# Performance work log

Hardware: AMD Instinct MI355X
Metric: run time of the kernel (lower is better)

## Reference

```python
import jax, jax.numpy as jnp
import numpy as np

D_MODEL = 1024
NUM_HEADS = 16
HEAD_DIM = D_MODEL // NUM_HEADS
ALPHA = 1.0


def setup_inputs() -> dict:
    key = jax.random.key(0)
    ks = jax.random.split(key, 9)
    B, T, D = 2, 2048, D_MODEL
    s = 1.0 / np.sqrt(D)
    inp = {
        "x": jax.random.normal(ks[0], (B, T, D), dtype=jnp.float32),
        "Wq": jax.random.uniform(ks[1], (D, D), jnp.float32, -s, s),
        "bq": jax.random.uniform(ks[2], (D,), jnp.float32, -s, s),
        "Wk": jax.random.uniform(ks[3], (D, D), jnp.float32, -s, s),
        "bk": jax.random.uniform(ks[4], (D,), jnp.float32, -s, s),
        "Wv": jax.random.uniform(ks[5], (D, D), jnp.float32, -s, s),
        "bv": jax.random.uniform(ks[6], (D,), jnp.float32, -s, s),
        "Wo": jax.random.uniform(ks[7], (D, D), jnp.float32, -s, s),
        "bo": jax.random.uniform(ks[8], (D,), jnp.float32, -s, s),
    }
    return inp


def reference(x, Wq, bq, Wk, bk, Wv, bv, Wo, bo):
    B, T, D = x.shape
    H, hd = NUM_HEADS, HEAD_DIM

    def split_heads(y):  # [B,T,D] -> [B,H,T,hd]
        return y.reshape(B, T, H, hd).transpose(0, 2, 1, 3)

    Q = split_heads(x @ Wq.T + bq)
    K = split_heads(x @ Wk.T + bk)
    V = split_heads(x @ Wv.T + bv)

    scores = jnp.einsum('bhid,bhjd->bhij', Q, K) / jnp.sqrt(jnp.float32(hd))

    t = jnp.arange(T)
    delta = t[:, None] - t[None, :]  # [T,T], i - j
    causal_mask = delta < 0          # j > i (strict upper triangle)
    # similarity_power_law decay bias: -(delta)^alpha for delta >= 0, else 0
    decay = jnp.where(causal_mask, 0.0, -(delta.astype(jnp.float32) ** ALPHA))

    scores = jnp.where(causal_mask, -jnp.inf, scores) + decay
    attn = jax.nn.softmax(scores, axis=-1)

    out = jnp.einsum('bhij,bhjd->bhid', attn, V)
    out = out.transpose(0, 2, 1, 3).reshape(B, T, D)
    return out @ Wo.T + bo
```

## Files before the change

### kernel.cpp

```cpp
#include <hip/hip_runtime.h>

#define TT 2048
#define DD 1024
#define HH 16
#define HD 64
#define NTOK 4096

typedef __bf16 bf16x8 __attribute__((ext_vector_type(8)));
typedef short short4v __attribute__((ext_vector_type(4)));
typedef float f32x4 __attribute__((ext_vector_type(4)));

__device__ __forceinline__ unsigned short f2bf(float f) {
  unsigned u = __float_as_uint(f);
  u += 0x7fffu + ((u >> 16) & 1u);
  return (unsigned short)(u >> 16);
}

#if __has_builtin(__builtin_amdgcn_mfma_f32_16x16x16bf16_1k)
__device__ __forceinline__ f32x4 mfma16(short4v a, short4v b, f32x4 c) {
  return __builtin_amdgcn_mfma_f32_16x16x16bf16_1k(a, b, c, 0, 0, 0);
}
#else
__device__ __forceinline__ f32x4 mfma16(short4v a, short4v b, f32x4 c) {
  asm("v_mfma_f32_16x16x16_bf16 %0, %1, %2, %0\n\ts_nop 7\n\ts_nop 7"
      : "+v"(c) : "v"(a), "v"(b));
  return c;
}
#endif

typedef void __attribute__((address_space(1))) as1_void;
typedef void __attribute__((address_space(3))) as3_void;
__device__ __forceinline__ void gl_lds16(const void* g, void* l) {
  __builtin_amdgcn_global_load_lds((as1_void*)g, (as3_void*)l, 16, 0, 0);
}

__global__ void wcmha_cast_bf16(const float4* __restrict__ src,
                                ushort4* __restrict__ dst, int n4) {
  int i = blockIdx.x * blockDim.x + threadIdx.x;
  if (i < n4) {
    float4 v = src[i];
    ushort4 o;
    o.x = f2bf(v.x); o.y = f2bf(v.y); o.z = f2bf(v.z); o.w = f2bf(v.w);
    dst[i] = o;
  }
}

#define BM 128
#define BN 64
#define BK 32

template <int MODE>
__global__ __launch_bounds__(256)
void wcmha_gemm(const unsigned short* __restrict__ X,
                const unsigned short* __restrict__ W,
                const float* __restrict__ bias,
                void* __restrict__ Y) {
  __shared__ unsigned short As[BM * BK];
  __shared__ unsigned short Bs[BN * BK];
  const int tid = threadIdx.x;
  const int wid = tid >> 6;
  const int lane = tid & 63;
  const int m = lane & 15, quad = lane >> 4;
  const int m0 = blockIdx.x * BM;
  const int n0 = blockIdx.y * BN;
  const int wm = (wid >> 1) * 64;
  const int wn = (wid & 1) * 32;

  const int ca0 = wid * 128 + lane;
  const int ca1 = ca0 + 64;
  const int cb  = wid * 64 + lane;
  const unsigned short* aga = X + (size_t)(m0 + (ca0 >> 2)) * DD + (ca0 & 3) * 8;
  const unsigned short* agb = X + (size_t)(m0 + (ca1 >> 2)) * DD + (ca1 & 3) * 8;
  const unsigned short* bga = W + (size_t)(n0 + (cb >> 2)) * DD + (cb & 3) * 8;
  unsigned short* lda = &As[wid * 1024];
  unsigned short* ldb = &As[wid * 1024 + 512];
  unsigned short* ldc = &Bs[wid * 512];

  f32x4 acc[4][2];
#pragma unroll
  for (int i = 0; i < 4; ++i)
#pragma unroll
    for (int j = 0; j < 2; ++j) acc[i][j] = (f32x4){0.f, 0.f, 0.f, 0.f};

  for (int k0 = 0; k0 < DD; k0 += BK) {
    gl_lds16(aga + k0, lda);
    gl_lds16(agb + k0, ldb);
    gl_lds16(bga + k0, ldc);
    __syncthreads();
    bf16x8 af[4], bf[2];
#pragma unroll
    for (int mi = 0; mi < 4; ++mi)
      af[mi] = *(const bf16x8*)&As[(wm + mi * 16 + m) * BK + quad * 8];
#pragma unroll
    for (int ni = 0; ni < 2; ++ni)
      bf[ni] = *(const bf16x8*)&Bs[(wn + ni * 16 + m) * BK + quad * 8];
#pragma unroll
    for (int mi = 0; mi < 4; ++mi)
#pragma unroll
      for (int ni = 0; ni < 2; ++ni)
        acc[mi][ni] = (MODE == 1)
            ? __builtin_amdgcn_mfma_f32_16x16x32_bf16(bf[ni], af[mi], acc[mi][ni], 0, 0, 0)
            : __builtin_amdgcn_mfma_f32_16x16x32_bf16(af[mi], bf[ni], acc[mi][ni], 0, 0, 0);
    __syncthreads();
  }

  if (MODE == 2) {
    float* dst = (float*)Y;
#pragma unroll
    for (int mi = 0; mi < 4; ++mi)
#pragma unroll
      for (int ni = 0; ni < 2; ++ni) {
        int col = n0 + wn + ni * 16 + m;
        float bb = bias[col];
#pragma unroll
        for (int r = 0; r < 4; ++r) {
          int row = m0 + wm + mi * 16 + quad * 4 + r;
          dst[(size_t)row * DD + col] = acc[mi][ni][r] + bb;
        }
      }
  } else if (MODE == 0) {
    unsigned short* dst = (unsigned short*)Y;
#pragma unroll
    for (int mi = 0; mi < 4; ++mi)
#pragma unroll
      for (int ni = 0; ni < 2; ++ni) {
        int col = n0 + wn + ni * 16 + m;
        int h = col >> 6, d = col & 63;
        float bb = bias[col];
#pragma unroll
        for (int r = 0; r < 4; ++r) {
          int row = m0 + wm + mi * 16 + quad * 4 + r;
          int b = row >> 11, t = row & (TT - 1);
          dst[((size_t)(b * HH + h) * TT + t) * HD + d] = f2bf(acc[mi][ni][r] + bb);
        }
      }
  } else {
    unsigned short* dst = (unsigned short*)Y;
#pragma unroll
    for (int mi = 0; mi < 4; ++mi)
#pragma unroll
      for (int ni = 0; ni < 2; ++ni) {
        int row = m0 + wm + mi * 16 + m;
        int b = row >> 11, t = row & (TT - 1);
#pragma unroll
        for (int r = 0; r < 4; ++r) {
          int col = n0 + wn + ni * 16 + quad * 4 + r;
          int h = col >> 6, d = col & 63;
          dst[((size_t)(b * HH + h) * HD + d) * TT + t] = f2bf(acc[mi][ni][r] + bias[col]);
        }
      }
  }
}

__global__ __launch_bounds__(256)
void wcmha_attn(const unsigned short* __restrict__ Qb,
                const unsigned short* __restrict__ Kb,
                const unsigned short* __restrict__ Vt,
                unsigned short* __restrict__ O) {
  const int wid = threadIdx.x >> 6, lane = threadIdx.x & 63;
  const int gw = (blockIdx.x << 2) + wid;
  const int qt = gw & 127, bh = gw >> 7;
  const int qbase = qt << 4;
  const int il = lane & 15, quad = lane >> 4;
  const int ig = qbase + il;

  const unsigned short* q_ptr = Qb + (size_t)bh * TT * HD;
  const unsigned short* k_ptr = Kb + (size_t)bh * TT * HD;
  const unsigned short* v_ptr = Vt + (size_t)bh * HD * TT;

  const bf16x8 qf0 = *(const bf16x8*)(q_ptr + (size_t)ig * HD + quad * 8);
  const bf16x8 qf1 = *(const bf16x8*)(q_ptr + (size_t)ig * HD + 32 + quad * 8);

  const int j0 = (qbase >= 48) ? qbase - 48 : 0;

  f32x4 st[4];
#pragma unroll
  for (int jt = 0; jt < 4; ++jt) {
    const unsigned short* kp = k_ptr + (size_t)(j0 + jt * 16 + il) * HD;
    bf16x8 k0 = *(const bf16x8*)(kp + quad * 8);
    bf16x8 k1 = *(const bf16x8*)(kp + 32 + quad * 8);
    f32x4 a = {0.f, 0.f, 0.f, 0.f};
    a = __builtin_amdgcn_mfma_f32_16x16x32_bf16(k0, qf0, a, 0, 0, 0);
    a = __builtin_amdgcn_mfma_f32_16x16x32_bf16(k1, qf1, a, 0, 0, 0);
    st[jt] = a;
  }

  float mloc = -3.0e38f;
#pragma unroll
  for (int jt = 0; jt < 4; ++jt)
#pragma unroll
    for (int r = 0; r < 4; ++r) {
      int jg = j0 + jt * 16 + quad * 4 + r;
      float v = (jg > ig) ? -3.0e38f : st[jt][r] * 0.125f - (float)(ig - jg);
      st[jt][r] = v;
      mloc = fmaxf(mloc, v);
    }
  mloc = fmaxf(mloc, __shfl_xor(mloc, 16));
  mloc = fmaxf(mloc, __shfl_xor(mloc, 32));

  float rs = 0.f;
  short4v pf[4];
#pragma unroll
  for (int jt = 0; jt < 4; ++jt)
#pragma unroll
    for (int r = 0; r < 4; ++r) {
      float p = __expf(st[jt][r] - mloc);
      rs += p;
      pf[jt][r] = (short)f2bf(p);
    }
  rs += __shfl_xor(rs, 16);
  rs += __shfl_xor(rs, 32);

  f32x4 o_acc[4];
#pragma unroll
  for (int nt = 0; nt < 4; ++nt) o_acc[nt] = (f32x4){0.f, 0.f, 0.f, 0.f};
#pragma unroll
  for (int jt = 0; jt < 4; ++jt)
#pragma unroll
    for (int nt = 0; nt < 4; ++nt) {
      short4v vf = *(const short4v*)(v_ptr + (size_t)(nt * 16 + il) * TT +
                                     j0 + jt * 16 + quad * 4);
      o_acc[nt] = mfma16(vf, pf[jt], o_acc[nt]);
    }

  const float inv_l = 1.f / rs;
  const int b = bh >> 4, hh = bh & 15;
  unsigned short* ob = O + ((size_t)(b * TT + ig)) * DD + hh * HD;
#pragma unroll
  for (int nt = 0; nt < 4; ++nt)
#pragma unroll
    for (int r = 0; r < 4; ++r)
      ob[nt * 16 + quad * 4 + r] = f2bf(o_acc[nt][r] * inv_l);
}

extern "C" void kernel_launch(void* const* d_in, const int* in_sizes, int n_in,
                              void* d_out, int out_size, void* d_ws, size_t ws_size,
                              hipStream_t stream) {
  const float* x  = (const float*)d_in[0];
  const float* Wq = (const float*)d_in[1];
  const float* bq = (const float*)d_in[2];
  const float* Wk = (const float*)d_in[3];
  const float* bk = (const float*)d_in[4];
  const float* Wv = (const float*)d_in[5];
  const float* bv = (const float*)d_in[6];
  const float* Wo = (const float*)d_in[7];
  const float* bo = (const float*)d_in[8];

  char* ws = (char*)d_ws;
  unsigned short* xb  = (unsigned short*)(ws);
  unsigned short* wqb = (unsigned short*)(ws + (8u << 20));
  unsigned short* wkb = wqb + (1u << 20);
  unsigned short* wvb = wkb + (1u << 20);
  unsigned short* wob = wvb + (1u << 20);
  unsigned short* Qb  = (unsigned short*)(ws + (16u << 20));
  unsigned short* Kb  = (unsigned short*)(ws + (24u << 20));
  unsigned short* Vt  = (unsigned short*)(ws + (32u << 20));
  unsigned short* Ob  = xb;

  wcmha_cast_bf16<<<4096, 256, 0, stream>>>((const float4*)x,  (ushort4*)xb,  NTOK * DD / 4);
  wcmha_cast_bf16<<<1024, 256, 0, stream>>>((const float4*)Wq, (ushort4*)wqb, DD * DD / 4);
  wcmha_cast_bf16<<<1024, 256, 0, stream>>>((const float4*)Wk, (ushort4*)wkb, DD * DD / 4);
  wcmha_cast_bf16<<<1024, 256, 0, stream>>>((const float4*)Wv, (ushort4*)wvb, DD * DD / 4);
  wcmha_cast_bf16<<<1024, 256, 0, stream>>>((const float4*)Wo, (ushort4*)wob, DD * DD / 4);

  dim3 gproj(NTOK / BM, DD / BN);
  wcmha_gemm<0><<<gproj, 256, 0, stream>>>(xb, wqb, bq, Qb);
  wcmha_gemm<0><<<gproj, 256, 0, stream>>>(xb, wkb, bk, Kb);
  wcmha_gemm<1><<<gproj, 256, 0, stream>>>(xb, wvb, bv, Vt);

  wcmha_attn<<<1024, 256, 0, stream>>>(Qb, Kb, Vt, Ob);

  wcmha_gemm<2><<<gproj, 256, 0, stream>>>(Ob, wob, bo, d_out);
}
```

Before: 186.6 us.

## Merge cast kernels, enlarge GEMM tiles to 128x128, fuse Q/K projections

All five fp32-to-bf16 casts now run in one launch, and the Q and K projections share a single launch. Every projection GEMM tile grows from 128x64 to 128x128 with 4x4 MFMA accumulators per wave, which raises arithmetic intensity and halves the block count. The goal is fewer kernel launches and less redundant operand loading. The trade-off is more accumulator registers per thread and fewer blocks (256 per GEMM), which may underfill the 256 CUs on MI355X.

```diff
diff --git a/kernel.cpp b/kernel.cpp
--- a/kernel.cpp
+++ b/kernel.cpp
@@ -5,6 +5,7 @@
 #define HH 16
 #define HD 64
 #define NTOK 4096
+#define BK 32
 
 typedef __bf16 bf16x8 __attribute__((ext_vector_type(8)));
 typedef short short4v __attribute__((ext_vector_type(4)));
@@ -34,122 +35,178 @@
   __builtin_amdgcn_global_load_lds((as1_void*)g, (as3_void*)l, 16, 0, 0);
 }
 
-__global__ void wcmha_cast_bf16(const float4* __restrict__ src,
-                                ushort4* __restrict__ dst, int n4) {
-  int i = blockIdx.x * blockDim.x + threadIdx.x;
-  if (i < n4) {
-    float4 v = src[i];
-    ushort4 o;
-    o.x = f2bf(v.x); o.y = f2bf(v.y); o.z = f2bf(v.z); o.w = f2bf(v.w);
-    dst[i] = o;
+__global__ __launch_bounds__(256)
+void wcmha_cast_all(const float4* __restrict__ x,  const float4* __restrict__ wq,
+                    const float4* __restrict__ wk, const float4* __restrict__ wv,
+                    const float4* __restrict__ wo,
+                    ushort4* __restrict__ xb,  ushort4* __restrict__ wqb,
+                    ushort4* __restrict__ wkb, ushort4* __restrict__ wvb,
+                    ushort4* __restrict__ wob) {
+  const int i = blockIdx.x * 256 + threadIdx.x;
+  const float4* src;
+  ushort4* dst;
+  int off;
+  if (i < 1048576) {
+    src = x; dst = xb; off = i;
+  } else {
+    int j = i - 1048576;
+    int sel = j >> 18;
+    off = j & 262143;
+    const float4* ws_[4] = {wq, wk, wv, wo};
+    ushort4* wd_[4] = {wqb, wkb, wvb, wob};
+    src = ws_[sel]; dst = wd_[sel];
   }
-}
-
-#define BM 128
-#define BN 64
-#define BK 32
-
-template <int MODE>
-__global__ __launch_bounds__(256)
-void wcmha_gemm(const unsigned short* __restrict__ X,
-                const unsigned short* __restrict__ W,
-                const float* __restrict__ bias,
-                void* __restrict__ Y) {
-  __shared__ unsigned short As[BM * BK];
-  __shared__ unsigned short Bs[BN * BK];
+  float4 v = src[off];
+  ushort4 o;
+  o.x = f2bf(v.x); o.y = f2bf(v.y); o.z = f2bf(v.z); o.w = f2bf(v.w);
+  dst[off] = o;
+}
+
+template <bool SWAP>
+__device__ __forceinline__ void gemm128_core(
+    const unsigned short* __restrict__ X, const unsigned short* __restrict__ W,
+    int m0, int n0, unsigned short* As, unsigned short* Bs, f32x4 acc[4][4]) {
   const int tid = threadIdx.x;
-  const int wid = tid >> 6;
-  const int lane = tid & 63;
+  const int wid = tid >> 6, lane = tid & 63;
   const int m = lane & 15, quad = lane >> 4;
-  const int m0 = blockIdx.x * BM;
-  const int n0 = blockIdx.y * BN;
-  const int wm = (wid >> 1) * 64;
-  const int wn = (wid & 1) * 32;
-
-  const int ca0 = wid * 128 + lane;
-  const int ca1 = ca0 + 64;
-  const int cb  = wid * 64 + lane;
-  const unsigned short* aga = X + (size_t)(m0 + (ca0 >> 2)) * DD + (ca0 & 3) * 8;
-  const unsigned short* agb = X + (size_t)(m0 + (ca1 >> 2)) * DD + (ca1 & 3) * 8;
-  const unsigned short* bga = W + (size_t)(n0 + (cb >> 2)) * DD + (cb & 3) * 8;
-  unsigned short* lda = &As[wid * 1024];
-  unsigned short* ldb = &As[wid * 1024 + 512];
-  unsigned short* ldc = &Bs[wid * 512];
-
-  f32x4 acc[4][2];
+  const int wm = (wid >> 1) * 64, wn = (wid & 1) * 64;
+
+  const int c0 = wid * 64 + lane;
+  const int c1 = c0 + 256;
+  const unsigned short* ga0 = X + (size_t)(m0 + (c0 >> 2)) * DD + (c0 & 3) * 8;
+  const unsigned short* ga1 = X + (size_t)(m0 + (c1 >> 2)) * DD + (c1 & 3) * 8;
+  const unsigned short* gb0 = W + (size_t)(n0 + (c0 >> 2)) * DD + (c0 & 3) * 8;
+  const unsigned short* gb1 = W + (size_t)(n0 + (c1 >> 2)) * DD + (c1 & 3) * 8;
+  unsigned short* la0 = As + wid * 512;
+  unsigned short* la1 = As + 2048 + wid * 512;
+  unsigned short* lb0 = Bs + wid * 512;
+  unsigned short* lb1 = Bs + 2048 + wid * 512;
+
 #pragma unroll
   for (int i = 0; i < 4; ++i)
 #pragma unroll
-    for (int j = 0; j < 2; ++j) acc[i][j] = (f32x4){0.f, 0.f, 0.f, 0.f};
+    for (int j = 0; j < 4; ++j) acc[i][j] = (f32x4){0.f, 0.f, 0.f, 0.f};
 
   for (int k0 = 0; k0 < DD; k0 += BK) {
-    gl_lds16(aga + k0, lda);
-    gl_lds16(agb + k0, ldb);
-    gl_lds16(bga + k0, ldc);
+    gl_lds16(ga0 + k0, la0);
+    gl_lds16(ga1 + k0, la1);
+    gl_lds16(gb0 + k0, lb0);
+    gl_lds16(gb1 + k0, lb1);
     __syncthreads();
-    bf16x8 af[4], bf[2];
+    bf16x8 af[4], bf[4];
 #pragma unroll
     for (int mi = 0; mi < 4; ++mi)
       af[mi] = *(const bf16x8*)&As[(wm + mi * 16 + m) * BK + quad * 8];
 #pragma unroll
-    for (int ni = 0; ni < 2; ++ni)
+    for (int ni = 0; ni < 4; ++ni)
       bf[ni] = *(const bf16x8*)&Bs[(wn + ni * 16 + m) * BK + quad * 8];
 #pragma unroll
     for (int mi = 0; mi < 4; ++mi)
 #pragma unroll
-      for (int ni = 0; ni < 2; ++ni)
-        acc[mi][ni] = (MODE == 1)
+      for (int ni = 0; ni < 4; ++ni)
+        acc[mi][ni] = SWAP
             ? __builtin_amdgcn_mfma_f32_16x16x32_bf16(bf[ni], af[mi], acc[mi][ni], 0, 0, 0)
             : __builtin_amdgcn_mfma_f32_16x16x32_bf16(af[mi], bf[ni], acc[mi][ni], 0, 0, 0);
     __syncthreads();
   }
-
-  if (MODE == 2) {
-    float* dst = (float*)Y;
-#pragma unroll
-    for (int mi = 0; mi < 4; ++mi)
-#pragma unroll
-      for (int ni = 0; ni < 2; ++ni) {
-        int col = n0 + wn + ni * 16 + m;
-        float bb = bias[col];
-#pragma unroll
-        for (int r = 0; r < 4; ++r) {
-          int row = m0 + wm + mi * 16 + quad * 4 + r;
-          dst[(size_t)row * DD + col] = acc[mi][ni][r] + bb;
-        }
+}
+
+__global__ __launch_bounds__(256)
+void wcmha_gemm_qk(const unsigned short* __restrict__ X,
+                   const unsigned short* __restrict__ Wq,
+                   const unsigned short* __restrict__ Wk,
+                   const float* __restrict__ bq, const float* __restrict__ bk,
+                   unsigned short* __restrict__ Qb, unsigned short* __restrict__ Kb) {
+  __shared__ unsigned short As[128 * BK];
+  __shared__ unsigned short Bs[128 * BK];
+  const int mat = blockIdx.y >> 3;
+  const int m0 = blockIdx.x * 128;
+  const int n0 = (blockIdx.y & 7) * 128;
+  const unsigned short* W = mat ? Wk : Wq;
+  const float* bias = mat ? bk : bq;
+  unsigned short* dst = mat ? Kb : Qb;
+
+  f32x4 acc[4][4];
+  gemm128_core<false>(X, W, m0, n0, As, Bs, acc);
+
+  const int lane = threadIdx.x & 63, wid = threadIdx.x >> 6;
+  const int m = lane & 15, quad = lane >> 4;
+  const int wm = (wid >> 1) * 64, wn = (wid & 1) * 64;
+#pragma unroll
+  for (int mi = 0; mi < 4; ++mi)
+#pragma unroll
+    for (int ni = 0; ni < 4; ++ni) {
+      int col = n0 + wn + ni * 16 + m;
+      int h = col >> 6, d = col & 63;
+      float bb = bias[col];
+#pragma unroll
+      for (int r = 0; r < 4; ++r) {
+        int row = m0 + wm + mi * 16 + quad * 4 + r;
+        int b = row >> 11, t = row & (TT - 1);
+        dst[((size_t)(b * HH + h) * TT + t) * HD + d] = f2bf(acc[mi][ni][r] + bb);
       }
-  } else if (MODE == 0) {
-    unsigned short* dst = (unsigned short*)Y;
-#pragma unroll
-    for (int mi = 0; mi < 4; ++mi)
-#pragma unroll
-      for (int ni = 0; ni < 2; ++ni) {
-        int col = n0 + wn + ni * 16 + m;
+    }
+}
+
+__global__ __launch_bounds__(256)
+void wcmha_gemm_v(const unsigned short* __restrict__ X,
+                  const unsigned short* __restrict__ W,
+                  const float* __restrict__ bias,
+                  unsigned short* __restrict__ Vt) {
+  __shared__ unsigned short As[128 * BK];
+  __shared__ unsigned short Bs[128 * BK];
+  const int m0 = blockIdx.x * 128;
+  const int n0 = blockIdx.y * 128;
+
+  f32x4 acc[4][4];
+  gemm128_core<true>(X, W, m0, n0, As, Bs, acc);
+
+  const int lane = threadIdx.x & 63, wid = threadIdx.x >> 6;
+  const int m = lane & 15, quad = lane >> 4;
+  const int wm = (wid >> 1) * 64, wn = (wid & 1) * 64;
+#pragma unroll
+  for (int mi = 0; mi < 4; ++mi) {
+    int row = m0 + wm + mi * 16 + m;
+    int b = row >> 11, t = row & (TT - 1);
+#pragma unroll
+    for (int ni = 0; ni < 4; ++ni)
+#pragma unroll
+      for (int r = 0; r < 4; ++r) {
+        int col = n0 + wn + ni * 16 + quad * 4 + r;
         int h = col >> 6, d = col & 63;
-        float bb = bias[col];
-#pragma unroll
-        for (int r = 0; r < 4; ++r) {
-          int row = m0 + wm + mi * 16 + quad * 4 + r;
-          int b = row >> 11, t = row & (TT - 1);
-          dst[((size_t)(b * HH + h) * TT + t) * HD + d] = f2bf(acc[mi][ni][r] + bb);
-        }
-      }
-  } else {
-    unsigned short* dst = (unsigned short*)Y;
-#pragma unroll
-    for (int mi = 0; mi < 4; ++mi)
-#pragma unroll
-      for (int ni = 0; ni < 2; ++ni) {
-        int row = m0 + wm + mi * 16 + m;
-        int b = row >> 11, t = row & (TT - 1);
-#pragma unroll
-        for (int r = 0; r < 4; ++r) {
-          int col = n0 + wn + ni * 16 + quad * 4 + r;
-          int h = col >> 6, d = col & 63;
-          dst[((size_t)(b * HH + h) * HD + d) * TT + t] = f2bf(acc[mi][ni][r] + bias[col]);
-        }
+        Vt[((size_t)(b * HH + h) * HD + d) * TT + t] = f2bf(acc[mi][ni][r] + bias[col]);
       }
   }
+}
+
+__global__ __launch_bounds__(256)
+void wcmha_gemm_out(const unsigned short* __restrict__ X,
+                    const unsigned short* __restrict__ W,
+                    const float* __restrict__ bias,
+                    float* __restrict__ Y) {
+  __shared__ unsigned short As[128 * BK];
+  __shared__ unsigned short Bs[128 * BK];
+  const int m0 = blockIdx.x * 128;
+  const int n0 = blockIdx.y * 128;
+
+  f32x4 acc[4][4];
+  gemm128_core<false>(X, W, m0, n0, As, Bs, acc);
+
+  const int lane = threadIdx.x & 63, wid = threadIdx.x >> 6;
+  const int m = lane & 15, quad = lane >> 4;
+  const int wm = (wid >> 1) * 64, wn = (wid & 1) * 64;
+#pragma unroll
+  for (int mi = 0; mi < 4; ++mi)
+#pragma unroll
+    for (int ni = 0; ni < 4; ++ni) {
+      int col = n0 + wn + ni * 16 + m;
+      float bb = bias[col];
+#pragma unroll
+      for (int r = 0; r < 4; ++r) {
+        int row = m0 + wm + mi * 16 + quad * 4 + r;
+        Y[(size_t)row * DD + col] = acc[mi][ni][r] + bb;
+      }
+    }
 }
 
 __global__ __launch_bounds__(256)
@@ -257,18 +314,15 @@
   unsigned short* Vt  = (unsigned short*)(ws + (32u << 20));
   unsigned short* Ob  = xb;
 
-  wcmha_cast_bf16<<<4096, 256, 0, stream>>>((const float4*)x,  (ushort4*)xb,  NTOK * DD / 4);
-  wcmha_cast_bf16<<<1024, 256, 0, stream>>>((const float4*)Wq, (ushort4*)wqb, DD * DD / 4);
-  wcmha_cast_bf16<<<1024, 256, 0, stream>>>((const float4*)Wk, (ushort4*)wkb, DD * DD / 4);
-  wcmha_cast_bf16<<<1024, 256, 0, stream>>>((const float4*)Wv, (ushort4*)wvb, DD * DD / 4);
-  wcmha_cast_bf16<<<1024, 256, 0, stream>>>((const float4*)Wo, (ushort4*)wob, DD * DD / 4);
-
-  dim3 gproj(NTOK / BM, DD / BN);
-  wcmha_gemm<0><<<gproj, 256, 0, stream>>>(xb, wqb, bq, Qb);
-  wcmha_gemm<0><<<gproj, 256, 0, stream>>>(xb, wkb, bk, Kb);
-  wcmha_gemm<1><<<gproj, 256, 0, stream>>>(xb, wvb, bv, Vt);
+  wcmha_cast_all<<<8192, 256, 0, stream>>>(
+      (const float4*)x, (const float4*)Wq, (const float4*)Wk,
+      (const float4*)Wv, (const float4*)Wo,
+      (ushort4*)xb, (ushort4*)wqb, (ushort4*)wkb, (ushort4*)wvb, (ushort4*)wob);
+
+  wcmha_gemm_qk<<<dim3(32, 16), 256, 0, stream>>>(xb, wqb, wkb, bq, bk, Qb, Kb);
+  wcmha_gemm_v<<<dim3(32, 8), 256, 0, stream>>>(xb, wvb, bv, Vt);
 
   wcmha_attn<<<1024, 256, 0, stream>>>(Qb, Kb, Vt, Ob);
 
-  wcmha_gemm<2><<<gproj, 256, 0, stream>>>(Ob, wob, bo, d_out);
-}
+  wcmha_gemm_out<<<dim3(32, 8), 256, 0, stream>>>(Ob, wob, bo, (float*)d_out);
+}
```

Result: faster. 176.6 us (-5.4%).
